# Kernel optimization log

Measured on AMD Instinct MI355X. Metric: run time of the kernel, lower is better.

The kernel has to match this reference:

```python
import jax, jax.numpy as jnp
import numpy as np
from collections import deque

N = 100_000
D = 128
E = 200_000


def _build_huffman(n):
    """Equal-weight Huffman pairing: leaves 0..n-1, internals n..2n-2."""
    parent = np.full(2 * n - 1, -1, np.int64)
    code = np.zeros(2 * n - 1, np.int64)
    q = deque(range(n))
    nxt = n
    while len(q) > 1:
        a = q.popleft(); b = q.popleft()
        parent[a] = nxt; parent[b] = nxt
        code[a] = 0; code[b] = 1
        q.append(nxt); nxt += 1
    return parent, code


def _leaf_paths(parent, code, n):
    """Padded root-ward paths per leaf: internal-node ids, signs (1-2*code), mask."""
    cur = np.arange(n)
    P, S, M = [], [], []
    while True:
        p = parent[cur]
        valid = p >= 0
        if not valid.any():
            break
        P.append(np.where(valid, p - n, 0))
        S.append(np.where(valid, 1 - 2 * code[cur], 0).astype(np.float32))
        M.append(valid.astype(np.float32))
        cur = np.where(valid, p, cur)
    return (np.stack(P, 1).astype(np.int64),
            np.stack(S, 1), np.stack(M, 1))


def setup_inputs() -> dict:
    key = jax.random.key(0)
    k1, k2, k3 = jax.random.split(key, 3)
    parent, code = _build_huffman(N)
    paths_np, signs_np, mask_np = _leaf_paths(parent, code, N)
    edges = jax.random.randint(k1, (E, 2), 0, N, dtype=jnp.int64)
    Z1 = jax.random.uniform(k2, (N, D), dtype=jnp.float32)
    Z2 = jax.random.uniform(k3, (N - 1, D), dtype=jnp.float32)
    return {
        "edges": edges,
        "Z1": Z1,
        "Z2": Z2,
        "paths": jnp.asarray(paths_np),
        "signs": jnp.asarray(signs_np),
        "mask": jnp.asarray(mask_np),
    }


def reference(edges, Z1, Z2, paths, signs, mask):
    # loss = -sum_{(u,v) in edges} log p(v | u) under hierarchical softmax:
    # tree walk on v, input vector Z1[u]; at each internal node p on v's path,
    # add log sigmoid(sign * <Z1[u], Z2[p]>).
    u = edges[:, 0]
    v = edges[:, 1]
    z = Z1[u]                     # [E, D]
    pth = paths[v].T              # [L, E]
    sgn = signs[v].T              # [L, E]
    mk = mask[v].T                # [L, E]

    def step(acc, xs):
        p, s, m = xs
        x = jnp.einsum('ed,ed->e', z, Z2[p])        # [E]
        return acc + jnp.sum(m * jax.nn.log_sigmoid(s * x)), None

    total, _ = jax.lax.scan(step, jnp.float32(0.0), (pth, sgn, mk))
    return -total
```

## Files before the change

### kernel.cpp

```cpp
#include <hip/hip_runtime.h>


typedef _Float16 half8 __attribute__((ext_vector_type(8)));
typedef _Float16 half2v __attribute__((ext_vector_type(2)));

__global__ __launch_bounds__(256) void dw_pack_f16(
    const float* __restrict__ src, _Float16* __restrict__ dst, int n8)
{
    const int i = blockIdx.x * 256 + threadIdx.x;
    if (i < n8) {
        const float4* s = (const float4*)src;
        const float4 a = s[2 * i];
        const float4 b = s[2 * i + 1];
        half8 h;
        h[0] = (_Float16)a.x; h[1] = (_Float16)a.y;
        h[2] = (_Float16)a.z; h[3] = (_Float16)a.w;
        h[4] = (_Float16)b.x; h[5] = (_Float16)b.y;
        h[6] = (_Float16)b.z; h[7] = (_Float16)b.w;
        ((half8*)dst)[i] = h;
    }
}

template <int LT>
__global__ __launch_bounds__(256) void dw_kernel_h(
    const int* __restrict__ edges,
    const float* __restrict__ Z1,
    const _Float16* __restrict__ Z2h,
    const int* __restrict__ paths,
    const float* __restrict__ signs,
    float* __restrict__ partials,
    int E, int L_rt)
{
    const int tid   = blockIdx.x * blockDim.x + threadIdx.x;
    const int group = tid >> 4;
    const int lane  = tid & 15;
    const int L     = (LT > 0) ? LT : L_rt;

    float acc = 0.0f;

    if (group < E) {
        const int e = group;
        const int u = edges[2 * e];
        const int v = edges[2 * e + 1];

        const float4* zr = (const float4*)(Z1 + (size_t)u * 128);
        const float4 za = zr[2 * lane];
        const float4 zb = zr[2 * lane + 1];

#if defined(__has_builtin) && __has_builtin(__builtin_amdgcn_fdot2)
        half2v zh[4];
        zh[0][0] = (_Float16)za.x; zh[0][1] = (_Float16)za.y;
        zh[1][0] = (_Float16)za.z; zh[1][1] = (_Float16)za.w;
        zh[2][0] = (_Float16)zb.x; zh[2][1] = (_Float16)zb.y;
        zh[3][0] = (_Float16)zb.z; zh[3][1] = (_Float16)zb.w;
#endif

        const int*   pr = paths + (size_t)v * L;
        const float* sr = signs + (size_t)v * L;

        float accm = 0.0f;
        float prod = 1.0f;

#pragma unroll
        for (int t = 0; t < L; ++t) {
            const int   p = pr[t];
            const float s = sr[t];

            union { half8 h8; half2v h2[4]; } w;
            w.h8 = ((const half8*)(Z2h + (size_t)p * 128))[lane];

            float d = 0.0f;
#if defined(__has_builtin) && __has_builtin(__builtin_amdgcn_fdot2)
            d = __builtin_amdgcn_fdot2(w.h2[0], zh[0], d, false);
            d = __builtin_amdgcn_fdot2(w.h2[1], zh[1], d, false);
            d = __builtin_amdgcn_fdot2(w.h2[2], zh[2], d, false);
            d = __builtin_amdgcn_fdot2(w.h2[3], zh[3], d, false);
#else
            d = fmaf((float)w.h8[0], za.x, d);
            d = fmaf((float)w.h8[1], za.y, d);
            d = fmaf((float)w.h8[2], za.z, d);
            d = fmaf((float)w.h8[3], za.w, d);
            d = fmaf((float)w.h8[4], zb.x, d);
            d = fmaf((float)w.h8[5], zb.y, d);
            d = fmaf((float)w.h8[6], zb.z, d);
            d = fmaf((float)w.h8[7], zb.w, d);
#endif

            d += __shfl_xor(d, 1);
            d += __shfl_xor(d, 2);
            d += __shfl_xor(d, 4);
            d += __shfl_xor(d, 8);

            const float y  = s * d;
            const float ex = __expf(-fabsf(y));
            prod = prod * fmaf(fabsf(s), ex, 1.0f);
            accm += fminf(y, 0.0f);
        }

        acc = accm - __logf(prod);
    }

    for (int off = 32; off >= 1; off >>= 1)
        acc += __shfl_down(acc, off);

    __shared__ float ws[4];
    const int wid = threadIdx.x >> 6;
    if ((threadIdx.x & 63) == 0) ws[wid] = acc;
    __syncthreads();
    if (threadIdx.x == 0)
        partials[blockIdx.x] = ws[0] + ws[1] + ws[2] + ws[3];
}

template <int LT>
__global__ __launch_bounds__(256) void dw_kernel_t(
    const int* __restrict__ edges,
    const float* __restrict__ Z1,
    const float* __restrict__ Z2,
    const int* __restrict__ paths,
    const float* __restrict__ signs,
    float* __restrict__ partials,
    int E, int L_rt)
{
    const int tid   = blockIdx.x * blockDim.x + threadIdx.x;
    const int group = tid >> 4;
    const int lane  = tid & 15;
    const int L     = (LT > 0) ? LT : L_rt;

    float acc = 0.0f;

    if (group < E) {
        const int e = group;
        const int u = edges[2 * e];
        const int v = edges[2 * e + 1];

        const float4* zr = (const float4*)(Z1 + (size_t)u * 128);
        const float4 za = zr[lane];
        const float4 zb = zr[lane + 16];

        const int*    pr  = paths + (size_t)v * L;
        const float*  sr  = signs + (size_t)v * L;
        const float4* Z2v = (const float4*)Z2;

        float accm = 0.0f;
        float prod = 1.0f;

#pragma unroll
        for (int t = 0; t < L; ++t) {
            const int   p = pr[t];
            const float s = sr[t];

            const float4 wa = Z2v[p * 32 + lane];
            const float4 wb = Z2v[p * 32 + lane + 16];

            float d = za.x * wa.x + za.y * wa.y + za.z * wa.z + za.w * wa.w
                    + zb.x * wb.x + zb.y * wb.y + zb.z * wb.z + zb.w * wb.w;

            d += __shfl_xor(d, 1);
            d += __shfl_xor(d, 2);
            d += __shfl_xor(d, 4);
            d += __shfl_xor(d, 8);

            const float y  = s * d;
            const float ex = __expf(-fabsf(y));
            prod = prod * fmaf(fabsf(s), ex, 1.0f);
            accm += fminf(y, 0.0f);
        }

        acc = accm - __logf(prod);
    }

    for (int off = 32; off >= 1; off >>= 1)
        acc += __shfl_down(acc, off);

    __shared__ float ws[4];
    const int wid = threadIdx.x >> 6;
    if ((threadIdx.x & 63) == 0) ws[wid] = acc;
    __syncthreads();
    if (threadIdx.x == 0)
        partials[blockIdx.x] = ws[0] + ws[1] + ws[2] + ws[3];
}

__global__ __launch_bounds__(1024) void dw_reduce(
    const float* __restrict__ partials, int n, float* __restrict__ out)
{
    float s = 0.0f;
    for (int i = threadIdx.x; i < n; i += 1024) s += partials[i];

    for (int off = 32; off >= 1; off >>= 1)
        s += __shfl_down(s, off);

    __shared__ float ws[16];
    const int wid = threadIdx.x >> 6;
    if ((threadIdx.x & 63) == 0) ws[wid] = s;
    __syncthreads();
    if (threadIdx.x == 0) {
        float b = 0.0f;
#pragma unroll
        for (int i = 0; i < 16; ++i) b += ws[i];
        out[0] = -b * 0.0625f;
    }
}

extern "C" void kernel_launch(void* const* d_in, const int* in_sizes, int n_in,
                              void* d_out, int out_size, void* d_ws, size_t ws_size,
                              hipStream_t stream)
{
    const int*   edges = (const int*)d_in[0];
    const float* Z1    = (const float*)d_in[1];
    const float* Z2    = (const float*)d_in[2];
    const int*   paths = (const int*)d_in[3];
    const float* signs = (const float*)d_in[4];
    float*       out   = (float*)d_out;

    const int E = in_sizes[0] / 2;
    const int D = in_sizes[1] - in_sizes[2];
    const int N = in_sizes[1] / D;
    const int L = in_sizes[3] / N;

    const int threads = 256;
    const int blocks  = (E * 16 + threads - 1) / threads;

    const size_t z2h_bytes = (size_t)in_sizes[2] * sizeof(_Float16);
    const size_t part_off  = (z2h_bytes + 255) & ~(size_t)255;
    const bool   use_f16   = (ws_size >= part_off + (size_t)blocks * 4) && (D == 128);

    if (use_f16) {
        _Float16* Z2h   = (_Float16*)d_ws;
        float*    parts = (float*)((char*)d_ws + part_off);

        const int n8 = in_sizes[2] / 8;
        dw_pack_f16<<<(n8 + 255) / 256, 256, 0, stream>>>(Z2, Z2h, n8);

        if (L == 17)
            dw_kernel_h<17><<<blocks, threads, 0, stream>>>(edges, Z1, Z2h, paths, signs, parts, E, L);
        else if (L == 16)
            dw_kernel_h<16><<<blocks, threads, 0, stream>>>(edges, Z1, Z2h, paths, signs, parts, E, L);
        else if (L == 18)
            dw_kernel_h<18><<<blocks, threads, 0, stream>>>(edges, Z1, Z2h, paths, signs, parts, E, L);
        else
            dw_kernel_h<0><<<blocks, threads, 0, stream>>>(edges, Z1, Z2h, paths, signs, parts, E, L);

        dw_reduce<<<1, 1024, 0, stream>>>(parts, blocks, out);
    } else {
        float* parts = (float*)d_ws;

        if (L == 17)
            dw_kernel_t<17><<<blocks, threads, 0, stream>>>(edges, Z1, Z2, paths, signs, parts, E, L);
        else if (L == 16)
            dw_kernel_t<16><<<blocks, threads, 0, stream>>>(edges, Z1, Z2, paths, signs, parts, E, L);
        else if (L == 18)
            dw_kernel_t<18><<<blocks, threads, 0, stream>>>(edges, Z1, Z2, paths, signs, parts, E, L);
        else
            dw_kernel_t<0><<<blocks, threads, 0, stream>>>(edges, Z1, Z2, paths, signs, parts, E, L);

        dw_reduce<<<1, 1024, 0, stream>>>(parts, blocks, out);
    }
}
```

Before: 204.7 us.

## Use 32-lane groups per edge with butterfly-transposed reduction over four path nodes

Each edge is now handled by 32 lanes instead of 16, and each lane loads 4 halves of a Z2 row instead of 8. Four path nodes are processed together using a transpose-style butterfly reduction, so each lane ends up owning one node's dot product and the shuffle count per node drops. The aim is more parallelism, shorter per-thread dependency chains and fewer shuffles. In exchange there are twice as many threads and smaller per-lane loads. Because each value is now accumulated across more lanes, the final scaling constants change, and the fp32 fallback path gets a matching 0.5 factor.

```diff
diff --git a/kernel.cpp b/kernel.cpp
--- a/kernel.cpp
+++ b/kernel.cpp
@@ -1,8 +1,16 @@
 #include <hip/hip_runtime.h>
 
 
-typedef _Float16 half8 __attribute__((ext_vector_type(8)));
+typedef _Float16 half8  __attribute__((ext_vector_type(8)));
+typedef _Float16 half4v __attribute__((ext_vector_type(4)));
 typedef _Float16 half2v __attribute__((ext_vector_type(2)));
+typedef float    floatx2 __attribute__((ext_vector_type(2)));
+
+#if defined(__has_builtin)
+#if __has_builtin(__builtin_amdgcn_fdot2)
+#define HAVE_FDOT2 1
+#endif
+#endif
 
 __global__ __launch_bounds__(256) void dw_pack_f16(
     const float* __restrict__ src, _Float16* __restrict__ dst, int n8)
@@ -21,8 +29,27 @@
     }
 }
 
+__device__ __forceinline__ float dw_dot4h(
+    const _Float16* __restrict__ Z2h, int p, int lane5,
+    half2v zh01, half2v zh23)
+{
+    union { half4v h4; half2v h2[2]; } w;
+    w.h4 = ((const half4v*)(Z2h + (size_t)(unsigned)p * 128))[lane5];
+#ifdef HAVE_FDOT2
+    float d = __builtin_amdgcn_fdot2(w.h2[0], zh01, 0.0f, false);
+    d = __builtin_amdgcn_fdot2(w.h2[1], zh23, d, false);
+    return d;
+#else
+    float d = (float)w.h4[0] * (float)zh01[0];
+    d = fmaf((float)w.h4[1], (float)zh01[1], d);
+    d = fmaf((float)w.h4[2], (float)zh23[0], d);
+    d = fmaf((float)w.h4[3], (float)zh23[1], d);
+    return d;
+#endif
+}
+
 template <int LT>
-__global__ __launch_bounds__(256) void dw_kernel_h(
+__global__ __launch_bounds__(256, 4) void dw_kernel32(
     const int* __restrict__ edges,
     const float* __restrict__ Z1,
     const _Float16* __restrict__ Z2h,
@@ -32,69 +59,73 @@
     int E, int L_rt)
 {
     const int tid   = blockIdx.x * blockDim.x + threadIdx.x;
-    const int group = tid >> 4;
-    const int lane  = tid & 15;
+    const int group = tid >> 5;
+    const int lane5 = tid & 31;
     const int L     = (LT > 0) ? LT : L_rt;
 
     float acc = 0.0f;
 
     if (group < E) {
-        const int e = group;
-        const int u = edges[2 * e];
-        const int v = edges[2 * e + 1];
-
-        const float4* zr = (const float4*)(Z1 + (size_t)u * 128);
-        const float4 za = zr[2 * lane];
-        const float4 zb = zr[2 * lane + 1];
-
-#if defined(__has_builtin) && __has_builtin(__builtin_amdgcn_fdot2)
-        half2v zh[4];
-        zh[0][0] = (_Float16)za.x; zh[0][1] = (_Float16)za.y;
-        zh[1][0] = (_Float16)za.z; zh[1][1] = (_Float16)za.w;
-        zh[2][0] = (_Float16)zb.x; zh[2][1] = (_Float16)zb.y;
-        zh[3][0] = (_Float16)zb.z; zh[3][1] = (_Float16)zb.w;
-#endif
+        const int u = edges[2 * group];
+        const int v = edges[2 * group + 1];
+
+        const float4 z4 = ((const float4*)(Z1 + (size_t)u * 128))[lane5];
+        half2v zh01, zh23;
+        zh01[0] = (_Float16)z4.x; zh01[1] = (_Float16)z4.y;
+        zh23[0] = (_Float16)z4.z; zh23[1] = (_Float16)z4.w;
 
         const int*   pr = paths + (size_t)v * L;
         const float* sr = signs + (size_t)v * L;
 
+        const bool b0 = lane5 & 1;
+        const bool b1 = lane5 & 2;
+        const int  own = lane5 & 3;
+
         float accm = 0.0f;
         float prod = 1.0f;
 
-#pragma unroll
-        for (int t = 0; t < L; ++t) {
+        int t = 0;
+#pragma unroll
+        for (; t + 4 <= L; t += 4) {
+            const int p0 = pr[t + 0], p1 = pr[t + 1];
+            const int p2 = pr[t + 2], p3 = pr[t + 3];
+            const float s = sr[t + own];
+
+            const float d0 = dw_dot4h(Z2h, p0, lane5, zh01, zh23);
+            const float d1 = dw_dot4h(Z2h, p1, lane5, zh01, zh23);
+            const float d2 = dw_dot4h(Z2h, p2, lane5, zh01, zh23);
+            const float d3 = dw_dot4h(Z2h, p3, lane5, zh01, zh23);
+
+            const float ua = b0 ? d0 : d1, ka = b0 ? d1 : d0;
+            const float av = ka + __shfl_xor(ua, 1);
+            const float ub = b0 ? d2 : d3, kb = b0 ? d3 : d2;
+            const float bv = kb + __shfl_xor(ub, 1);
+            const float uc = b1 ? av : bv, kc = b1 ? bv : av;
+            float cv = kc + __shfl_xor(uc, 2);
+            cv += __shfl_xor(cv, 4);
+            cv += __shfl_xor(cv, 8);
+            cv += __shfl_xor(cv, 16);
+
+            const float y  = s * cv;
+            const float ex = __expf(-fabsf(y));
+            prod = prod * fmaf(fabsf(s), ex, 1.0f);
+            accm += fminf(y, 0.0f);
+        }
+#pragma unroll
+        for (; t < L; ++t) {
             const int   p = pr[t];
             const float s = sr[t];
-
-            union { half8 h8; half2v h2[4]; } w;
-            w.h8 = ((const half8*)(Z2h + (size_t)p * 128))[lane];
-
-            float d = 0.0f;
-#if defined(__has_builtin) && __has_builtin(__builtin_amdgcn_fdot2)
-            d = __builtin_amdgcn_fdot2(w.h2[0], zh[0], d, false);
-            d = __builtin_amdgcn_fdot2(w.h2[1], zh[1], d, false);
-            d = __builtin_amdgcn_fdot2(w.h2[2], zh[2], d, false);
-            d = __builtin_amdgcn_fdot2(w.h2[3], zh[3], d, false);
-#else
-            d = fmaf((float)w.h8[0], za.x, d);
-            d = fmaf((float)w.h8[1], za.y, d);
-            d = fmaf((float)w.h8[2], za.z, d);
-            d = fmaf((float)w.h8[3], za.w, d);
-            d = fmaf((float)w.h8[4], zb.x, d);
-            d = fmaf((float)w.h8[5], zb.y, d);
-            d = fmaf((float)w.h8[6], zb.z, d);
-            d = fmaf((float)w.h8[7], zb.w, d);
-#endif
-
+            float d = dw_dot4h(Z2h, p, lane5, zh01, zh23);
             d += __shfl_xor(d, 1);
             d += __shfl_xor(d, 2);
             d += __shfl_xor(d, 4);
             d += __shfl_xor(d, 8);
-
+            d += __shfl_xor(d, 16);
             const float y  = s * d;
             const float ex = __expf(-fabsf(y));
-            prod = prod * fmaf(fabsf(s), ex, 1.0f);
-            accm += fminf(y, 0.0f);
+            const float m  = (lane5 < 8) ? 1.0f : 0.0f;
+            prod = prod * fmaf(m * fabsf(s), ex, 1.0f);
+            accm += m * fminf(y, 0.0f);
         }
 
         acc = accm - __logf(prod);
@@ -129,9 +160,8 @@
     float acc = 0.0f;
 
     if (group < E) {
-        const int e = group;
-        const int u = edges[2 * e];
-        const int v = edges[2 * e + 1];
+        const int u = edges[2 * group];
+        const int v = edges[2 * group + 1];
 
         const float4* zr = (const float4*)(Z1 + (size_t)u * 128);
         const float4 za = zr[lane];
@@ -166,7 +196,7 @@
             accm += fminf(y, 0.0f);
         }
 
-        acc = accm - __logf(prod);
+        acc = (accm - __logf(prod)) * 0.5f;
     }
 
     for (int off = 32; off >= 1; off >>= 1)
@@ -197,7 +227,7 @@
         float b = 0.0f;
 #pragma unroll
         for (int i = 0; i < 16; ++i) b += ws[i];
-        out[0] = -b * 0.0625f;
+        out[0] = -b * 0.125f;
     }
 }
 
@@ -217,14 +247,15 @@
     const int N = in_sizes[1] / D;
     const int L = in_sizes[3] / N;
 
-    const int threads = 256;
-    const int blocks  = (E * 16 + threads - 1) / threads;
-
-    const size_t z2h_bytes = (size_t)in_sizes[2] * sizeof(_Float16);
+    const int threads  = 256;
+    const int blocks32 = (E * 32 + threads - 1) / threads;
+    const int blocks16 = (E * 16 + threads - 1) / threads;
+
+    const size_t z2h_bytes = (size_t)in_sizes[2] * 2;
     const size_t part_off  = (z2h_bytes + 255) & ~(size_t)255;
-    const bool   use_f16   = (ws_size >= part_off + (size_t)blocks * 4) && (D == 128);
-
-    if (use_f16) {
+    const bool   use_h     = (ws_size >= part_off + (size_t)blocks32 * 4) && (D == 128);
+
+    if (use_h) {
         _Float16* Z2h   = (_Float16*)d_ws;
         float*    parts = (float*)((char*)d_ws + part_off);
 
@@ -232,27 +263,25 @@
         dw_pack_f16<<<(n8 + 255) / 256, 256, 0, stream>>>(Z2, Z2h, n8);
 
         if (L == 17)
-            dw_kernel_h<17><<<blocks, threads, 0, stream>>>(edges, Z1, Z2h, paths, signs, parts, E, L);
+            dw_kernel32<17><<<blocks32, threads, 0, stream>>>(edges, Z1, Z2h, paths, signs, parts, E, L);
         else if (L == 16)
-            dw_kernel_h<16><<<blocks, threads, 0, stream>>>(edges, Z1, Z2h, paths, signs, parts, E, L);
+            dw_kernel32<16><<<blocks32, threads, 0, stream>>>(edges, Z1, Z2h, paths, signs, parts, E, L);
         else if (L == 18)
-            dw_kernel_h<18><<<blocks, threads, 0, stream>>>(edges, Z1, Z2h, paths, signs, parts, E, L);
+            dw_kernel32<18><<<blocks32, threads, 0, stream>>>(edges, Z1, Z2h, paths, signs, parts, E, L);
         else
-            dw_kernel_h<0><<<blocks, threads, 0, stream>>>(edges, Z1, Z2h, paths, signs, parts, E, L);
-
-        dw_reduce<<<1, 1024, 0, stream>>>(parts, blocks, out);
+            dw_kernel32<0><<<blocks32, threads, 0, stream>>>(edges, Z1, Z2h, paths, signs, parts, E, L);
+
+        dw_reduce<<<1, 1024, 0, stream>>>(parts, blocks32, out);
     } else {
         float* parts = (float*)d_ws;
-
         if (L == 17)
-            dw_kernel_t<17><<<blocks, threads, 0, stream>>>(edges, Z1, Z2, paths, signs, parts, E, L);
+            dw_kernel_t<17><<<blocks16, threads, 0, stream>>>(edges, Z1, Z2, paths, signs, parts, E, L);
         else if (L == 16)
-            dw_kernel_t<16><<<blocks, threads, 0, stream>>>(edges, Z1, Z2, paths, signs, parts, E, L);
+            dw_kernel_t<16><<<blocks16, threads, 0, stream>>>(edges, Z1, Z2, paths, signs, parts, E, L);
         else if (L == 18)
-            dw_kernel_t<18><<<blocks, threads, 0, stream>>>(edges, Z1, Z2, paths, signs, parts, E, L);
+            dw_kernel_t<18><<<blocks16, threads, 0, stream>>>(edges, Z1, Z2, paths, signs, parts, E, L);
         else
-            dw_kernel_t<0><<<blocks, threads, 0, stream>>>(edges, Z1, Z2, paths, signs, parts, E, L);
-
-        dw_reduce<<<1, 1024, 0, stream>>>(parts, blocks, out);
-    }
-}
+            dw_kernel_t<0><<<blocks16, threads, 0, stream>>>(edges, Z1, Z2, paths, signs, parts, E, L);
+        dw_reduce<<<1, 1024, 0, stream>>>(parts, blocks16, out);
+    }
+}
```

Result: slower. 228.5 us (+11.6%).
